# Kernel optimization log

Measured on AMD Instinct MI355X. Metric: run time of the kernel, lower is better.

The kernel has to match this reference:

```python
import jax, jax.numpy as jnp
import numpy as np

B, N, D, H = 2, 2048, 1024, 16
DH = D // H
SCALE = DH ** -0.5

def setup_inputs() -> dict:
    key = jax.random.key(0)
    k1, k2, k3 = jax.random.split(key, 3)
    x = jax.random.normal(k1, (B, N, D), dtype=jnp.float32)
    W_qkv = jax.random.normal(k2, (3 * D, D), dtype=jnp.float32) * (D ** -0.5)
    W_out = jax.random.normal(k3, (D, D), dtype=jnp.float32) * (D ** -0.5)
    mask = jnp.tril(jnp.ones((N, N), dtype=jnp.int32))  # causal mask; 0 -> -inf
    return {"x": x, "mask": mask, "W_qkv": W_qkv, "W_out": W_out}

def reference(x, mask, W_qkv, W_out):
    b, n, d = x.shape
    qkv = x @ W_qkv.T                                   # [B,N,3D]
    qkv = qkv.reshape(b, n, 3, H, DH).transpose(2, 0, 3, 1, 4)  # [3,B,H,N,DH]
    q, k, v = qkv[0], qkv[1], qkv[2]
    attn = jnp.einsum('bhqd,bhkd->bhqk', q, k) * SCALE  # [B,H,N,N]
    attn = jnp.where(mask == 0, -jnp.inf, attn)
    attn = jax.nn.softmax(attn, axis=-1)
    out = jnp.einsum('bhqk,bhkd->bhqd', attn, v)        # [B,H,N,DH]
    out = out.transpose(0, 2, 1, 3).reshape(b, n, d)    # [B,N,D]
    return out @ W_out.T
```

## Files before the change

### kernel.cpp

```cpp
#include <hip/hip_runtime.h>
#include <hip/hip_bf16.h>


typedef __hip_bfloat16 bf16;
typedef short bf16x8 __attribute__((ext_vector_type(8)));
typedef short bf16x4 __attribute__((ext_vector_type(4)));
typedef float f32x4 __attribute__((ext_vector_type(4)));

#define QSCALE 0.1803368801111204f

typedef __attribute__((address_space(3))) unsigned int lds_u32;
typedef const __attribute__((address_space(1))) unsigned int glob_u32;

__device__ __forceinline__ void glds16(const void* g, void* l) {
    __builtin_amdgcn_global_load_lds((glob_u32*)g, (lds_u32*)l, 16, 0, 0);
}

__device__ __forceinline__ short f2bf(float f) {
    __hip_bfloat16 h = __float2bfloat16(f);
    return *reinterpret_cast<short*>(&h);
}

__device__ __forceinline__ unsigned pack_bf16(float a, float b) {
    unsigned au = __builtin_bit_cast(unsigned, a) + 0x8000u;
    unsigned bu = __builtin_bit_cast(unsigned, b) + 0x8000u;
    return __builtin_amdgcn_perm(bu, au, 0x07060302u);
}

__global__ void cast4(const float* __restrict__ src, bf16* __restrict__ dst, int n4) {
    int i = blockIdx.x * blockDim.x + threadIdx.x;
    if (i < n4) {
        float4 f = reinterpret_cast<const float4*>(src)[i];
        short4 s;
        s.x = f2bf(f.x); s.y = f2bf(f.y); s.z = f2bf(f.z); s.w = f2bf(f.w);
        reinterpret_cast<short4*>(dst)[i] = s;
    }
}

template<int EPI>
__global__ __launch_bounds__(256)
void gemm128(const bf16* __restrict__ A, const bf16* __restrict__ Bt,
             float* __restrict__ Cf,
             bf16* __restrict__ qp, bf16* __restrict__ kp, bf16* __restrict__ vp,
             int K, int Ncols) {
    __shared__ alignas(16) short As[2][4096];
    __shared__ alignas(16) short Bs[2][4096];

    const int tid = threadIdx.x;
    const int wave = tid >> 6, lane = tid & 63;
    const int quad = lane >> 4, l16 = lane & 15;
    const int wm = wave >> 1, wn = wave & 1;
    const int m0 = blockIdx.x * 128;
    const int n0 = blockIdx.y * 128;

    f32x4 acc[4][4] = {};

    const int srow = tid >> 2;
    const int skk  = (((tid & 3) ^ ((tid >> 3) & 3))) * 8;
    const bf16* Ag = A  + (size_t)(m0 + srow) * K + skk;
    const bf16* Bg = Bt + (size_t)(n0 + srow) * K + skk;
    const size_t rowskip = (size_t)64 * K;
    short* Asl = &As[0][0] + tid * 8;
    short* Bsl = &Bs[0][0] + tid * 8;

    const int xk = (quad ^ ((l16 >> 1) & 3)) * 8;
    const int arow = wm * 64 + l16;
    const int brow = wn * 64 + l16;

    const int KI = K >> 5;
    glds16(Ag, Asl);
    glds16(Ag + rowskip, Asl + 2048);
    glds16(Bg, Bsl);
    glds16(Bg + rowskip, Bsl + 2048);
    __syncthreads();

    int buf = 0;
    for (int ki = 0; ki < KI; ++ki) {
        if (ki + 1 < KI) {
            const bf16* ag = Ag + (ki + 1) * 32;
            const bf16* bg = Bg + (ki + 1) * 32;
            short* ad = Asl + (buf ^ 1) * 4096;
            short* bd = Bsl + (buf ^ 1) * 4096;
            glds16(ag, ad);
            glds16(ag + rowskip, ad + 2048);
            glds16(bg, bd);
            glds16(bg + rowskip, bd + 2048);
        }
        const short* ab = &As[buf][0];
        const short* bb = &Bs[buf][0];
        bf16x8 af[4], bf[4];
        #pragma unroll
        for (int mt = 0; mt < 4; ++mt)
            af[mt] = *reinterpret_cast<const bf16x8*>(ab + (arow + mt * 16) * 32 + xk);
        #pragma unroll
        for (int nt = 0; nt < 4; ++nt)
            bf[nt] = *reinterpret_cast<const bf16x8*>(bb + (brow + nt * 16) * 32 + xk);
        #pragma unroll
        for (int mt = 0; mt < 4; ++mt)
            #pragma unroll
            for (int nt = 0; nt < 4; ++nt)
                acc[mt][nt] = __builtin_amdgcn_mfma_f32_16x16x32_bf16(
                    af[mt], bf[nt], acc[mt][nt], 0, 0, 0);
        __syncthreads();
        buf ^= 1;
    }

    #pragma unroll
    for (int mt = 0; mt < 4; ++mt) {
        #pragma unroll
        for (int nt = 0; nt < 4; ++nt) {
            #pragma unroll
            for (int r = 0; r < 4; ++r) {
                int gm = m0 + wm * 64 + mt * 16 + quad * 4 + r;
                int gn = n0 + wn * 64 + nt * 16 + l16;
                float val = acc[mt][nt][r];
                if (EPI == 0) {
                    int sel = gn >> 10, rem = gn & 1023;
                    int h = rem >> 6, dh = rem & 63;
                    int b = gm >> 11, nq = gm & 2047;
                    if (sel == 0) val *= QSCALE;
                    bf16* dst = (sel == 0) ? qp : ((sel == 1) ? kp : vp);
                    dst[((((size_t)b * 16 + h) * 2048) + nq) * 64 + dh] = __float2bfloat16(val);
                } else {
                    Cf[(size_t)gm * Ncols + gn] = val;
                }
            }
        }
    }
}

__global__ __launch_bounds__(256)
void flash_attn(const bf16* __restrict__ Q, const bf16* __restrict__ K,
                const bf16* __restrict__ V, bf16* __restrict__ O) {
    __shared__ alignas(16) short Ks[2][64][72];
    __shared__ alignas(16) short Vt[2][64][68];

    const int tid = threadIdx.x;
    const int wave = tid >> 6, lane = tid & 63;
    const int quad = lane >> 4, l16 = lane & 15;
    const int bh = blockIdx.x;
    const int yy = blockIdx.y;
    const int g = yy & 7, kq = yy >> 3;
    const int qt = (kq == 0) ? g : (kq == 1) ? (15 - g) : (kq == 2) ? (16 + g) : (31 - g);
    const int q0 = qt * 64;
    const float NEG_INF = -__builtin_inff();

    const bf16* Qb = Q + (size_t)bh * 2048 * 64;
    const bf16* Kb = K + (size_t)bh * 2048 * 64;
    const bf16* Vb = V + (size_t)bh * 2048 * 64;

    const int qrow = q0 + wave * 16 + l16;
    const bf16x8 qf0 = *reinterpret_cast<const bf16x8*>(Qb + (size_t)qrow * 64 + quad * 8);
    const bf16x8 qf1 = *reinterpret_cast<const bf16x8*>(Qb + (size_t)qrow * 64 + 32 + quad * 8);

    float l_part = 0.f;
    f32x4 o[4] = {};

    const int krow = tid >> 2;
    const int kcol = (tid & 3) * 16;
    const int kb = (tid & 15) * 4;
    const int db = (tid >> 4) * 4;

    {
        bf16x8 a0 = *reinterpret_cast<const bf16x8*>(Kb + (size_t)krow * 64 + kcol);
        bf16x8 a1 = *reinterpret_cast<const bf16x8*>(Kb + (size_t)krow * 64 + kcol + 8);
        bf16x4 L0 = *reinterpret_cast<const bf16x4*>(Vb + (size_t)(kb + 0) * 64 + db);
        bf16x4 L1 = *reinterpret_cast<const bf16x4*>(Vb + (size_t)(kb + 1) * 64 + db);
        bf16x4 L2 = *reinterpret_cast<const bf16x4*>(Vb + (size_t)(kb + 2) * 64 + db);
        bf16x4 L3 = *reinterpret_cast<const bf16x4*>(Vb + (size_t)(kb + 3) * 64 + db);
        *reinterpret_cast<bf16x8*>(&Ks[0][krow][kcol]) = a0;
        *reinterpret_cast<bf16x8*>(&Ks[0][krow][kcol + 8]) = a1;
        #pragma unroll
        for (int j = 0; j < 4; ++j) {
            bf16x4 w; w[0] = L0[j]; w[1] = L1[j]; w[2] = L2[j]; w[3] = L3[j];
            *reinterpret_cast<bf16x4*>(&Vt[0][db + j][kb]) = w;
        }
    }
    __syncthreads();

    int buf = 0;
    for (int j0 = 0; j0 < q0; j0 += 64) {
        const bf16* Kn = Kb + (size_t)(j0 + 64) * 64;
        const bf16* Vn = Vb + (size_t)(j0 + 64) * 64;
        bf16x8 nk0 = *reinterpret_cast<const bf16x8*>(Kn + (size_t)krow * 64 + kcol);
        bf16x8 nk1 = *reinterpret_cast<const bf16x8*>(Kn + (size_t)krow * 64 + kcol + 8);
        bf16x4 N0 = *reinterpret_cast<const bf16x4*>(Vn + (size_t)(kb + 0) * 64 + db);
        bf16x4 N1 = *reinterpret_cast<const bf16x4*>(Vn + (size_t)(kb + 1) * 64 + db);
        bf16x4 N2 = *reinterpret_cast<const bf16x4*>(Vn + (size_t)(kb + 2) * 64 + db);
        bf16x4 N3 = *reinterpret_cast<const bf16x4*>(Vn + (size_t)(kb + 3) * 64 + db);

        f32x4 s[4];
        #pragma unroll
        for (int t = 0; t < 4; ++t) {
            bf16x8 k0 = *reinterpret_cast<const bf16x8*>(&Ks[buf][16 * t + l16][quad * 8]);
            bf16x8 k1 = *reinterpret_cast<const bf16x8*>(&Ks[buf][16 * t + l16][32 + quad * 8]);
            f32x4 a = {};
            a = __builtin_amdgcn_mfma_f32_16x16x32_bf16(k0, qf0, a, 0, 0, 0);
            a = __builtin_amdgcn_mfma_f32_16x16x32_bf16(k1, qf1, a, 0, 0, 0);
            s[t] = a;
        }

        bf16x4 pk[4];
        #pragma unroll
        for (int t = 0; t < 4; ++t) {
            float p0 = __builtin_amdgcn_exp2f(s[t][0]);
            float p1 = __builtin_amdgcn_exp2f(s[t][1]);
            float p2 = __builtin_amdgcn_exp2f(s[t][2]);
            float p3 = __builtin_amdgcn_exp2f(s[t][3]);
            l_part += (p0 + p1) + (p2 + p3);
            unsigned* pku = reinterpret_cast<unsigned*>(&pk[t]);
            pku[0] = pack_bf16(p0, p1);
            pku[1] = pack_bf16(p2, p3);
        }

        #pragma unroll
        for (int t = 0; t < 4; ++t) {
            #pragma unroll
            for (int dt = 0; dt < 4; ++dt) {
                bf16x4 vf = *reinterpret_cast<const bf16x4*>(
                    &Vt[buf][dt * 16 + l16][t * 16 + quad * 4]);
                o[dt] = __builtin_amdgcn_mfma_f32_16x16x16bf16_1k(vf, pk[t], o[dt], 0, 0, 0);
            }
        }

        *reinterpret_cast<bf16x8*>(&Ks[buf ^ 1][krow][kcol]) = nk0;
        *reinterpret_cast<bf16x8*>(&Ks[buf ^ 1][krow][kcol + 8]) = nk1;
        #pragma unroll
        for (int j = 0; j < 4; ++j) {
            bf16x4 w; w[0] = N0[j]; w[1] = N1[j]; w[2] = N2[j]; w[3] = N3[j];
            *reinterpret_cast<bf16x4*>(&Vt[buf ^ 1][db + j][kb]) = w;
        }
        __syncthreads();
        buf ^= 1;
    }

    {
        f32x4 s[4];
        #pragma unroll
        for (int t = 0; t < 4; ++t) {
            if (t <= wave) {
                bf16x8 k0 = *reinterpret_cast<const bf16x8*>(&Ks[buf][16 * t + l16][quad * 8]);
                bf16x8 k1 = *reinterpret_cast<const bf16x8*>(&Ks[buf][16 * t + l16][32 + quad * 8]);
                f32x4 a = {};
                a = __builtin_amdgcn_mfma_f32_16x16x32_bf16(k0, qf0, a, 0, 0, 0);
                a = __builtin_amdgcn_mfma_f32_16x16x32_bf16(k1, qf1, a, 0, 0, 0);
                if (t == wave) {
                    #pragma unroll
                    for (int r = 0; r < 4; ++r)
                        if (quad * 4 + r > l16) a[r] = NEG_INF;
                }
                s[t] = a;
            }
        }
        bf16x4 pk[4];
        #pragma unroll
        for (int t = 0; t < 4; ++t) {
            if (t <= wave) {
                float p0 = __builtin_amdgcn_exp2f(s[t][0]);
                float p1 = __builtin_amdgcn_exp2f(s[t][1]);
                float p2 = __builtin_amdgcn_exp2f(s[t][2]);
                float p3 = __builtin_amdgcn_exp2f(s[t][3]);
                l_part += (p0 + p1) + (p2 + p3);
                unsigned* pku = reinterpret_cast<unsigned*>(&pk[t]);
                pku[0] = pack_bf16(p0, p1);
                pku[1] = pack_bf16(p2, p3);
            }
        }
        #pragma unroll
        for (int t = 0; t < 4; ++t) {
            if (t <= wave) {
                #pragma unroll
                for (int dt = 0; dt < 4; ++dt) {
                    bf16x4 vf = *reinterpret_cast<const bf16x4*>(
                        &Vt[buf][dt * 16 + l16][t * 16 + quad * 4]);
                    o[dt] = __builtin_amdgcn_mfma_f32_16x16x16bf16_1k(vf, pk[t], o[dt], 0, 0, 0);
                }
            }
        }
    }

    float l = l_part;
    l += __shfl_xor(l, 16, 64);
    l += __shfl_xor(l, 32, 64);
    const float inv = 1.f / l;

    const int b = bh >> 4, h = bh & 15;
    bf16* orow = O + ((size_t)b * 2048 + qrow) * 1024 + h * 64;
    #pragma unroll
    for (int dt = 0; dt < 4; ++dt) {
        bf16x4 w;
        unsigned* wu = reinterpret_cast<unsigned*>(&w);
        wu[0] = pack_bf16(o[dt][0] * inv, o[dt][1] * inv);
        wu[1] = pack_bf16(o[dt][2] * inv, o[dt][3] * inv);
        *reinterpret_cast<bf16x4*>(orow + dt * 16 + quad * 4) = w;
    }
}

extern "C" void kernel_launch(void* const* d_in, const int* in_sizes, int n_in,
                              void* d_out, int out_size, void* d_ws, size_t ws_size,
                              hipStream_t stream) {
    const float* x    = (const float*)d_in[0];
    const float* Wqkv = (const float*)d_in[2];
    const float* Wout = (const float*)d_in[3];
    float* out = (float*)d_out;

    char* ws = (char*)d_ws;
    bf16* x_bf    = (bf16*)(ws);
    bf16* wqkv_bf = (bf16*)(ws + 8388608);
    bf16* wout_bf = (bf16*)(ws + 14680064);
    bf16* q       = (bf16*)(ws + 16777216);
    bf16* k       = (bf16*)(ws + 25165824);
    bf16* v       = (bf16*)(ws + 33554432);
    bf16* ao      = (bf16*)(ws + 41943040);

    cast4<<<4096, 256, 0, stream>>>(x, x_bf, 1048576);
    cast4<<<3072, 256, 0, stream>>>(Wqkv, wqkv_bf, 786432);
    cast4<<<1024, 256, 0, stream>>>(Wout, wout_bf, 262144);

    gemm128<0><<<dim3(32, 24), 256, 0, stream>>>(x_bf, wqkv_bf, nullptr, q, k, v, 1024, 3072);
    flash_attn<<<dim3(32, 32), 256, 0, stream>>>(q, k, v, ao);
    gemm128<1><<<dim3(32, 8), 256, 0, stream>>>(ao, wout_bf, out, nullptr, nullptr, nullptr, 1024, 1024);
}
```

Before: 189.2 us.

## Process two 64-row query tiles per attention block to reuse K/V tiles

Each flash-attention workgroup now handles 128 query rows: two 64-row sub-tiles (A and B) that share every K/V tile loaded into LDS. The diagonal is split into two extra steps with separate causal masking for each sub-tile, and the grid's y dimension is halved. This halves the K/V global loads and LDS staging per unit of query work and doubles the MFMA work per barrier. In exchange it doubles accumulator registers, which may lower occupancy, and leaves fewer blocks (512) to balance the causal workload.

Result: faster. 181.5 us (-4.1%).

```diff
diff --git a/kernel.cpp b/kernel.cpp
--- a/kernel.cpp
+++ b/kernel.cpp
@@ -140,21 +140,23 @@
     const int quad = lane >> 4, l16 = lane & 15;
     const int bh = blockIdx.x;
     const int yy = blockIdx.y;
-    const int g = yy & 7, kq = yy >> 3;
-    const int qt = (kq == 0) ? g : (kq == 1) ? (15 - g) : (kq == 2) ? (16 + g) : (31 - g);
-    const int q0 = qt * 64;
+    const int qt = (yy < 8) ? yy : (15 - (yy & 7));
+    const int Q0 = qt * 128;
     const float NEG_INF = -__builtin_inff();
 
     const bf16* Qb = Q + (size_t)bh * 2048 * 64;
     const bf16* Kb = K + (size_t)bh * 2048 * 64;
     const bf16* Vb = V + (size_t)bh * 2048 * 64;
 
-    const int qrow = q0 + wave * 16 + l16;
-    const bf16x8 qf0 = *reinterpret_cast<const bf16x8*>(Qb + (size_t)qrow * 64 + quad * 8);
-    const bf16x8 qf1 = *reinterpret_cast<const bf16x8*>(Qb + (size_t)qrow * 64 + 32 + quad * 8);
-
-    float l_part = 0.f;
-    f32x4 o[4] = {};
+    const int qrowA = Q0 + wave * 16 + l16;
+    const int qrowB = qrowA + 64;
+    const bf16x8 qfA0 = *reinterpret_cast<const bf16x8*>(Qb + (size_t)qrowA * 64 + quad * 8);
+    const bf16x8 qfA1 = *reinterpret_cast<const bf16x8*>(Qb + (size_t)qrowA * 64 + 32 + quad * 8);
+    const bf16x8 qfB0 = *reinterpret_cast<const bf16x8*>(Qb + (size_t)qrowB * 64 + quad * 8);
+    const bf16x8 qfB1 = *reinterpret_cast<const bf16x8*>(Qb + (size_t)qrowB * 64 + 32 + quad * 8);
+
+    float lA = 0.f, lB = 0.f;
+    f32x4 oA[4] = {}, oB[4] = {};
 
     const int krow = tid >> 2;
     const int kcol = (tid & 3) * 16;
@@ -179,7 +181,7 @@
     __syncthreads();
 
     int buf = 0;
-    for (int j0 = 0; j0 < q0; j0 += 64) {
+    for (int j0 = 0; j0 < Q0; j0 += 64) {
         const bf16* Kn = Kb + (size_t)(j0 + 64) * 64;
         const bf16* Vn = Vb + (size_t)(j0 + 64) * 64;
         bf16x8 nk0 = *reinterpret_cast<const bf16x8*>(Kn + (size_t)krow * 64 + kcol);
@@ -189,28 +191,30 @@
         bf16x4 N2 = *reinterpret_cast<const bf16x4*>(Vn + (size_t)(kb + 2) * 64 + db);
         bf16x4 N3 = *reinterpret_cast<const bf16x4*>(Vn + (size_t)(kb + 3) * 64 + db);
 
-        f32x4 s[4];
+        bf16x4 pkA[4], pkB[4];
         #pragma unroll
         for (int t = 0; t < 4; ++t) {
             bf16x8 k0 = *reinterpret_cast<const bf16x8*>(&Ks[buf][16 * t + l16][quad * 8]);
             bf16x8 k1 = *reinterpret_cast<const bf16x8*>(&Ks[buf][16 * t + l16][32 + quad * 8]);
-            f32x4 a = {};
-            a = __builtin_amdgcn_mfma_f32_16x16x32_bf16(k0, qf0, a, 0, 0, 0);
-            a = __builtin_amdgcn_mfma_f32_16x16x32_bf16(k1, qf1, a, 0, 0, 0);
-            s[t] = a;
-        }
-
-        bf16x4 pk[4];
-        #pragma unroll
-        for (int t = 0; t < 4; ++t) {
-            float p0 = __builtin_amdgcn_exp2f(s[t][0]);
-            float p1 = __builtin_amdgcn_exp2f(s[t][1]);
-            float p2 = __builtin_amdgcn_exp2f(s[t][2]);
-            float p3 = __builtin_amdgcn_exp2f(s[t][3]);
-            l_part += (p0 + p1) + (p2 + p3);
-            unsigned* pku = reinterpret_cast<unsigned*>(&pk[t]);
-            pku[0] = pack_bf16(p0, p1);
-            pku[1] = pack_bf16(p2, p3);
+            f32x4 sA = {}, sB = {};
+            sA = __builtin_amdgcn_mfma_f32_16x16x32_bf16(k0, qfA0, sA, 0, 0, 0);
+            sA = __builtin_amdgcn_mfma_f32_16x16x32_bf16(k1, qfA1, sA, 0, 0, 0);
+            sB = __builtin_amdgcn_mfma_f32_16x16x32_bf16(k0, qfB0, sB, 0, 0, 0);
+            sB = __builtin_amdgcn_mfma_f32_16x16x32_bf16(k1, qfB1, sB, 0, 0, 0);
+            float a0 = __builtin_amdgcn_exp2f(sA[0]);
+            float a1 = __builtin_amdgcn_exp2f(sA[1]);
+            float a2 = __builtin_amdgcn_exp2f(sA[2]);
+            float a3 = __builtin_amdgcn_exp2f(sA[3]);
+            float b0 = __builtin_amdgcn_exp2f(sB[0]);
+            float b1 = __builtin_amdgcn_exp2f(sB[1]);
+            float b2 = __builtin_amdgcn_exp2f(sB[2]);
+            float b3 = __builtin_amdgcn_exp2f(sB[3]);
+            lA += (a0 + a1) + (a2 + a3);
+            lB += (b0 + b1) + (b2 + b3);
+            unsigned* pa = reinterpret_cast<unsigned*>(&pkA[t]);
+            pa[0] = pack_bf16(a0, a1); pa[1] = pack_bf16(a2, a3);
+            unsigned* pb = reinterpret_cast<unsigned*>(&pkB[t]);
+            pb[0] = pack_bf16(b0, b1); pb[1] = pack_bf16(b2, b3);
         }
 
         #pragma unroll
@@ -219,7 +223,8 @@
             for (int dt = 0; dt < 4; ++dt) {
                 bf16x4 vf = *reinterpret_cast<const bf16x4*>(
                     &Vt[buf][dt * 16 + l16][t * 16 + quad * 4]);
-                o[dt] = __builtin_amdgcn_mfma_f32_16x16x16bf16_1k(vf, pk[t], o[dt], 0, 0, 0);
+                oA[dt] = __builtin_amdgcn_mfma_f32_16x16x16bf16_1k(vf, pkA[t], oA[dt], 0, 0, 0);
+                oB[dt] = __builtin_amdgcn_mfma_f32_16x16x16bf16_1k(vf, pkB[t], oB[dt], 0, 0, 0);
             }
         }
 
@@ -235,35 +240,93 @@
     }
 
     {
-        f32x4 s[4];
+        const bf16* Kn = Kb + (size_t)(Q0 + 64) * 64;
+        const bf16* Vn = Vb + (size_t)(Q0 + 64) * 64;
+        bf16x8 nk0 = *reinterpret_cast<const bf16x8*>(Kn + (size_t)krow * 64 + kcol);
+        bf16x8 nk1 = *reinterpret_cast<const bf16x8*>(Kn + (size_t)krow * 64 + kcol + 8);
+        bf16x4 N0 = *reinterpret_cast<const bf16x4*>(Vn + (size_t)(kb + 0) * 64 + db);
+        bf16x4 N1 = *reinterpret_cast<const bf16x4*>(Vn + (size_t)(kb + 1) * 64 + db);
+        bf16x4 N2 = *reinterpret_cast<const bf16x4*>(Vn + (size_t)(kb + 2) * 64 + db);
+        bf16x4 N3 = *reinterpret_cast<const bf16x4*>(Vn + (size_t)(kb + 3) * 64 + db);
+
+        bf16x4 pkA[4], pkB[4];
+        #pragma unroll
+        for (int t = 0; t < 4; ++t) {
+            bf16x8 k0 = *reinterpret_cast<const bf16x8*>(&Ks[buf][16 * t + l16][quad * 8]);
+            bf16x8 k1 = *reinterpret_cast<const bf16x8*>(&Ks[buf][16 * t + l16][32 + quad * 8]);
+            f32x4 sB = {};
+            sB = __builtin_amdgcn_mfma_f32_16x16x32_bf16(k0, qfB0, sB, 0, 0, 0);
+            sB = __builtin_amdgcn_mfma_f32_16x16x32_bf16(k1, qfB1, sB, 0, 0, 0);
+            float b0 = __builtin_amdgcn_exp2f(sB[0]);
+            float b1 = __builtin_amdgcn_exp2f(sB[1]);
+            float b2 = __builtin_amdgcn_exp2f(sB[2]);
+            float b3 = __builtin_amdgcn_exp2f(sB[3]);
+            lB += (b0 + b1) + (b2 + b3);
+            unsigned* pb = reinterpret_cast<unsigned*>(&pkB[t]);
+            pb[0] = pack_bf16(b0, b1); pb[1] = pack_bf16(b2, b3);
+            if (t <= wave) {
+                f32x4 sA = {};
+                sA = __builtin_amdgcn_mfma_f32_16x16x32_bf16(k0, qfA0, sA, 0, 0, 0);
+                sA = __builtin_amdgcn_mfma_f32_16x16x32_bf16(k1, qfA1, sA, 0, 0, 0);
+                if (t == wave) {
+                    #pragma unroll
+                    for (int r = 0; r < 4; ++r)
+                        if (quad * 4 + r > l16) sA[r] = NEG_INF;
+                }
+                float a0 = __builtin_amdgcn_exp2f(sA[0]);
+                float a1 = __builtin_amdgcn_exp2f(sA[1]);
+                float a2 = __builtin_amdgcn_exp2f(sA[2]);
+                float a3 = __builtin_amdgcn_exp2f(sA[3]);
+                lA += (a0 + a1) + (a2 + a3);
+                unsigned* pa = reinterpret_cast<unsigned*>(&pkA[t]);
+                pa[0] = pack_bf16(a0, a1); pa[1] = pack_bf16(a2, a3);
+            }
+        }
+        #pragma unroll
+        for (int t = 0; t < 4; ++t) {
+            #pragma unroll
+            for (int dt = 0; dt < 4; ++dt) {
+                bf16x4 vf = *reinterpret_cast<const bf16x4*>(
+                    &Vt[buf][dt * 16 + l16][t * 16 + quad * 4]);
+                oB[dt] = __builtin_amdgcn_mfma_f32_16x16x16bf16_1k(vf, pkB[t], oB[dt], 0, 0, 0);
+                if (t <= wave)
+                    oA[dt] = __builtin_amdgcn_mfma_f32_16x16x16bf16_1k(vf, pkA[t], oA[dt], 0, 0, 0);
+            }
+        }
+
+        *reinterpret_cast<bf16x8*>(&Ks[buf ^ 1][krow][kcol]) = nk0;
+        *reinterpret_cast<bf16x8*>(&Ks[buf ^ 1][krow][kcol + 8]) = nk1;
+        #pragma unroll
+        for (int j = 0; j < 4; ++j) {
+            bf16x4 w; w[0] = N0[j]; w[1] = N1[j]; w[2] = N2[j]; w[3] = N3[j];
+            *reinterpret_cast<bf16x4*>(&Vt[buf ^ 1][db + j][kb]) = w;
+        }
+        __syncthreads();
+        buf ^= 1;
+    }
+
+    {
+        bf16x4 pkB[4];
         #pragma unroll
         for (int t = 0; t < 4; ++t) {
             if (t <= wave) {
                 bf16x8 k0 = *reinterpret_cast<const bf16x8*>(&Ks[buf][16 * t + l16][quad * 8]);
                 bf16x8 k1 = *reinterpret_cast<const bf16x8*>(&Ks[buf][16 * t + l16][32 + quad * 8]);
-                f32x4 a = {};
-                a = __builtin_amdgcn_mfma_f32_16x16x32_bf16(k0, qf0, a, 0, 0, 0);
-                a = __builtin_amdgcn_mfma_f32_16x16x32_bf16(k1, qf1, a, 0, 0, 0);
+                f32x4 sB = {};
+                sB = __builtin_amdgcn_mfma_f32_16x16x32_bf16(k0, qfB0, sB, 0, 0, 0);
+                sB = __builtin_amdgcn_mfma_f32_16x16x32_bf16(k1, qfB1, sB, 0, 0, 0);
                 if (t == wave) {
                     #pragma unroll
                     for (int r = 0; r < 4; ++r)
-                        if (quad * 4 + r > l16) a[r] = NEG_INF;
+                        if (quad * 4 + r > l16) sB[r] = NEG_INF;
                 }
-                s[t] = a;
-            }
-        }
-        bf16x4 pk[4];
-        #pragma unroll
-        for (int t = 0; t < 4; ++t) {
-            if (t <= wave) {
-                float p0 = __builtin_amdgcn_exp2f(s[t][0]);
-                float p1 = __builtin_amdgcn_exp2f(s[t][1]);
-                float p2 = __builtin_amdgcn_exp2f(s[t][2]);
-                float p3 = __builtin_amdgcn_exp2f(s[t][3]);
-                l_part += (p0 + p1) + (p2 + p3);
-                unsigned* pku = reinterpret_cast<unsigned*>(&pk[t]);
-                pku[0] = pack_bf16(p0, p1);
-                pku[1] = pack_bf16(p2, p3);
+                float b0 = __builtin_amdgcn_exp2f(sB[0]);
+                float b1 = __builtin_amdgcn_exp2f(sB[1]);
+                float b2 = __builtin_amdgcn_exp2f(sB[2]);
+                float b3 = __builtin_amdgcn_exp2f(sB[3]);
+                lB += (b0 + b1) + (b2 + b3);
+                unsigned* pb = reinterpret_cast<unsigned*>(&pkB[t]);
+                pb[0] = pack_bf16(b0, b1); pb[1] = pack_bf16(b2, b3);
             }
         }
         #pragma unroll
@@ -273,26 +336,33 @@
                 for (int dt = 0; dt < 4; ++dt) {
                     bf16x4 vf = *reinterpret_cast<const bf16x4*>(
                         &Vt[buf][dt * 16 + l16][t * 16 + quad * 4]);
-                    o[dt] = __builtin_amdgcn_mfma_f32_16x16x16bf16_1k(vf, pk[t], o[dt], 0, 0, 0);
+                    oB[dt] = __builtin_amdgcn_mfma_f32_16x16x16bf16_1k(vf, pkB[t], oB[dt], 0, 0, 0);
                 }
             }
         }
     }
 
-    float l = l_part;
-    l += __shfl_xor(l, 16, 64);
-    l += __shfl_xor(l, 32, 64);
-    const float inv = 1.f / l;
+    lA += __shfl_xor(lA, 16, 64);
+    lA += __shfl_xor(lA, 32, 64);
+    lB += __shfl_xor(lB, 16, 64);
+    lB += __shfl_xor(lB, 32, 64);
+    const float invA = 1.f / lA;
+    const float invB = 1.f / lB;
 
     const int b = bh >> 4, h = bh & 15;
-    bf16* orow = O + ((size_t)b * 2048 + qrow) * 1024 + h * 64;
+    bf16* orowA = O + ((size_t)b * 2048 + qrowA) * 1024 + h * 64;
+    bf16* orowB = O + ((size_t)b * 2048 + qrowB) * 1024 + h * 64;
     #pragma unroll
     for (int dt = 0; dt < 4; ++dt) {
-        bf16x4 w;
-        unsigned* wu = reinterpret_cast<unsigned*>(&w);
-        wu[0] = pack_bf16(o[dt][0] * inv, o[dt][1] * inv);
-        wu[1] = pack_bf16(o[dt][2] * inv, o[dt][3] * inv);
-        *reinterpret_cast<bf16x4*>(orow + dt * 16 + quad * 4) = w;
+        bf16x4 wA, wB;
+        unsigned* ua = reinterpret_cast<unsigned*>(&wA);
+        ua[0] = pack_bf16(oA[dt][0] * invA, oA[dt][1] * invA);
+        ua[1] = pack_bf16(oA[dt][2] * invA, oA[dt][3] * invA);
+        *reinterpret_cast<bf16x4*>(orowA + dt * 16 + quad * 4) = wA;
+        unsigned* ub = reinterpret_cast<unsigned*>(&wB);
+        ub[0] = pack_bf16(oB[dt][0] * invB, oB[dt][1] * invB);
+        ub[1] = pack_bf16(oB[dt][2] * invB, oB[dt][3] * invB);
+        *reinterpret_cast<bf16x4*>(orowB + dt * 16 + quad * 4) = wB;
     }
 }
 
@@ -318,6 +388,6 @@
     cast4<<<1024, 256, 0, stream>>>(Wout, wout_bf, 262144);
 
     gemm128<0><<<dim3(32, 24), 256, 0, stream>>>(x_bf, wqkv_bf, nullptr, q, k, v, 1024, 3072);
-    flash_attn<<<dim3(32, 32), 256, 0, stream>>>(q, k, v, ao);
+    flash_attn<<<dim3(32, 16), 256, 0, stream>>>(q, k, v, ao);
     gemm128<1><<<dim3(32, 8), 256, 0, stream>>>(ao, wout_bf, out, nullptr, nullptr, nullptr, 1024, 1024);
 }
```
